# Kernel tuning notes

Hardware: AMD Instinct MI355X
Metric: run time of the kernel (lower is better)

Reference implementation:

```python
import jax, jax.numpy as jnp
import numpy as np

B, IN, HS, OUT, NBDA = 128, 64, 500, 10, 1


def setup_inputs() -> dict:
    key = jax.random.key(0)
    ks = jax.random.split(key, 16)
    inp = {
        "inputs": jax.random.normal(ks[0], (B, IN), jnp.float32),
        "hidden": jax.random.normal(ks[1], (B, HS), jnp.float32),
        "hebb": jax.random.uniform(ks[2], (B, HS, HS), jnp.float32),
        "et": jax.random.uniform(ks[3], (B, HS, HS), jnp.float32),
        "pw": jax.random.uniform(ks[4], (B, HS, HS), jnp.float32),
        # parameters (xavier-ish scale for linears, matching torch init magnitudes)
        "i2h_w": jax.random.normal(ks[5], (HS, IN), jnp.float32) * (1.0 / np.sqrt(IN)),
        "i2h_b": jnp.zeros((HS,), jnp.float32),
        "w": 0.01 * jax.random.uniform(ks[6], (HS, HS), jnp.float32),
        "alpha": 0.01 * jax.random.uniform(ks[7], (HS, HS), jnp.float32),
        "eta": 0.1 * jnp.ones((1,), jnp.float32),
        "etaet": 0.1 * jnp.ones((1,), jnp.float32),
        "h2DA_w": jax.random.normal(ks[8], (NBDA, HS), jnp.float32) * (1.0 / np.sqrt(HS)),
        "h2DA_b": jnp.zeros((NBDA,), jnp.float32),
        "h2o_w": jax.random.normal(ks[9], (OUT, HS), jnp.float32) * (1.0 / np.sqrt(HS)),
        "h2o_b": jnp.zeros((OUT,), jnp.float32),
        "h2v_w": jax.random.normal(ks[10], (1, HS), jnp.float32) * (1.0 / np.sqrt(HS)),
        "h2v_b": jnp.zeros((1,), jnp.float32),
    }
    return inp


def reference(inputs, hidden, hebb, et, pw,
              i2h_w, i2h_b, w, alpha, eta, etaet,
              h2DA_w, h2DA_b, h2o_w, h2o_b, h2v_w, h2v_b):
    # hactiv = tanh(i2h(x) + (w + alpha*pw) @ hidden)   [B,HS]
    pre = inputs @ i2h_w.T + i2h_b                       # [B,HS]
    rec = jnp.einsum('bij,bj->bi', w[None] + alpha[None] * pw, hidden)
    hactiv = jnp.tanh(pre + rec)

    activout = hactiv @ h2o_w.T + h2o_b                  # [B,OUT]
    valueout = hactiv @ h2v_w.T + h2v_b                  # [B,1]
    DAout = jnp.tanh(hactiv @ h2DA_w.T + h2DA_b)         # [B,1] (NBDA=1)

    # outer-product Hebbian trace update
    deltahebb = hactiv[:, :, None] * hidden[:, None, :]  # [B,HS,HS]
    deltapw = DAout.reshape(-1, 1, 1) * et               # retroactive modulation
    pw_new = jnp.clip(pw + deltapw, -1.0, 1.0)           # fully_modulated=True path
    hebb_new = hebb                                      # untouched when fully modulated
    et_new = (1.0 - etaet) * et + etaet * deltahebb
    hidden_new = hactiv

    return activout, valueout, hidden_new, hebb_new, et_new, pw_new
```

## Files before the change

### kernel.cpp

```cpp
#include <hip/hip_runtime.h>
#include <math.h>

#define B   128
#define IN  64
#define HS  500
#define OUT 10

typedef float f4 __attribute__((ext_vector_type(4)));

__global__ __launch_bounds__(256)
void k_hactiv(const float* __restrict__ inputs,
              const float* __restrict__ hidden,
              const float* __restrict__ pw,
              const float* __restrict__ i2h_w,
              const float* __restrict__ i2h_b,
              const float* __restrict__ w,
              const float* __restrict__ alpha,
              float* __restrict__ hactiv,
              float* __restrict__ hidden_new)
{
    __shared__ f4 h_lds[HS / 4];
    const int b    = blockIdx.x / (HS / 4);
    const int tile = blockIdx.x % (HS / 4);
    const int lane = threadIdx.x & 63;
    const int wv   = threadIdx.x >> 6;
    const int i    = tile * 4 + wv;

    if (threadIdx.x < HS / 4)
        h_lds[threadIdx.x] = ((const f4*)(hidden + (size_t)b * HS))[threadIdx.x];
    __syncthreads();

    const f4* __restrict__ pwrow = (const f4*)(pw + ((size_t)b * HS + i) * HS);
    const f4* __restrict__ wrow  = (const f4*)(w + (size_t)i * HS);
    const f4* __restrict__ arow  = (const f4*)(alpha + (size_t)i * HS);

    float acc = 0.f;
    #pragma unroll 2
    for (int v = lane; v < HS / 4; v += 64) {
        const f4 pv  = pwrow[v];
        const f4 wv4 = wrow[v];
        const f4 av  = arow[v];
        const f4 hv  = h_lds[v];
        acc += (wv4.x + av.x * pv.x) * hv.x
             + (wv4.y + av.y * pv.y) * hv.y
             + (wv4.z + av.z * pv.z) * hv.z
             + (wv4.w + av.w * pv.w) * hv.w;
    }

    acc += inputs[b * IN + lane] * i2h_w[i * IN + lane];

    #pragma unroll
    for (int off = 32; off > 0; off >>= 1)
        acc += __shfl_down(acc, off, 64);

    if (lane == 0) {
        float v = tanhf(acc + i2h_b[i]);
        hactiv[b * HS + i]     = v;
        hidden_new[b * HS + i] = v;
    }
}

__global__ __launch_bounds__(256)
void k_heads(const float* __restrict__ hactiv,
             const float* __restrict__ h2o_w,
             const float* __restrict__ h2o_b,
             const float* __restrict__ h2v_w,
             const float* __restrict__ h2v_b,
             const float* __restrict__ h2DA_w,
             const float* __restrict__ h2DA_b,
             float* __restrict__ activout,
             float* __restrict__ valueout,
             float* __restrict__ DAout)
{
    __shared__ float h_lds[HS];
    const int b    = blockIdx.x;
    const int lane = threadIdx.x & 63;
    const int wv   = threadIdx.x >> 6;

    for (int j = threadIdx.x; j < HS; j += 256) h_lds[j] = hactiv[b * HS + j];
    __syncthreads();

    float acc[3] = {0.f, 0.f, 0.f};
    #pragma unroll
    for (int oo = 0; oo < 3; ++oo) {
        const int o = wv * 3 + oo;
        const float* __restrict__ wr =
            (o < OUT) ? (h2o_w + (size_t)o * HS) : ((o == OUT) ? h2v_w : h2DA_w);
        float a = 0.f;
        for (int j = lane; j < HS; j += 64) a += wr[j] * h_lds[j];
        acc[oo] = a;
    }
    #pragma unroll
    for (int off = 32; off > 0; off >>= 1) {
        #pragma unroll
        for (int oo = 0; oo < 3; ++oo)
            acc[oo] += __shfl_down(acc[oo], off, 64);
    }
    if (lane == 0) {
        #pragma unroll
        for (int oo = 0; oo < 3; ++oo) {
            const int o = wv * 3 + oo;
            if (o < OUT)          activout[b * OUT + o] = acc[oo] + h2o_b[o];
            else if (o == OUT)    valueout[b]           = acc[oo] + h2v_b[0];
            else                  DAout[b]              = tanhf(acc[oo] + h2DA_b[0]);
        }
    }
}

#define NV4 (HS * HS / 4)

__global__ __launch_bounds__(256)
void k_update(const f4* __restrict__ hebb,
              const f4* __restrict__ et,
              const f4* __restrict__ pw,
              const float* __restrict__ hactiv,
              const float* __restrict__ hidden,
              const float* __restrict__ DAout,
              const float* __restrict__ etaet_p,
              f4* __restrict__ hebb_new,
              f4* __restrict__ et_new,
              f4* __restrict__ pw_new)
{
    const int   b     = blockIdx.y;
    const float etaet = etaet_p[0];
    const float omete = 1.f - etaet;
    const float da    = DAout[b];
    const size_t base = (size_t)b * NV4;

    const float* __restrict__ harow = hactiv + (size_t)b * HS;
    const f4*    __restrict__ hrow  = (const f4*)(hidden + (size_t)b * HS);

    const int stride = gridDim.x * blockDim.x;
    for (int v = blockIdx.x * blockDim.x + threadIdx.x; v < NV4; v += stride) {
        const int i  = v / (HS / 4);
        const int j4 = v - i * (HS / 4);

        const float ha = harow[i] * etaet;
        const f4 hj = hrow[j4];
        const f4 e  = __builtin_nontemporal_load(et + base + v);
        const f4 p  = pw[base + v];
        const f4 hb = __builtin_nontemporal_load(hebb + base + v);

        f4 en, pn;
        en.x = omete * e.x + ha * hj.x;
        en.y = omete * e.y + ha * hj.y;
        en.z = omete * e.z + ha * hj.z;
        en.w = omete * e.w + ha * hj.w;

        pn.x = fminf(fmaxf(p.x + da * e.x, -1.f), 1.f);
        pn.y = fminf(fmaxf(p.y + da * e.y, -1.f), 1.f);
        pn.z = fminf(fmaxf(p.z + da * e.z, -1.f), 1.f);
        pn.w = fminf(fmaxf(p.w + da * e.w, -1.f), 1.f);

        __builtin_nontemporal_store(hb, hebb_new + base + v);
        __builtin_nontemporal_store(en, et_new + base + v);
        __builtin_nontemporal_store(pn, pw_new + base + v);
    }
}

extern "C" void kernel_launch(void* const* d_in, const int* in_sizes, int n_in,
                              void* d_out, int out_size, void* d_ws, size_t ws_size,
                              hipStream_t stream) {
    const float* inputs  = (const float*)d_in[0];
    const float* hidden  = (const float*)d_in[1];
    const float* hebb    = (const float*)d_in[2];
    const float* et      = (const float*)d_in[3];
    const float* pw      = (const float*)d_in[4];
    const float* i2h_w   = (const float*)d_in[5];
    const float* i2h_b   = (const float*)d_in[6];
    const float* w       = (const float*)d_in[7];
    const float* alpha   = (const float*)d_in[8];
    const float* etaet   = (const float*)d_in[10];
    const float* h2DA_w  = (const float*)d_in[11];
    const float* h2DA_b  = (const float*)d_in[12];
    const float* h2o_w   = (const float*)d_in[13];
    const float* h2o_b   = (const float*)d_in[14];
    const float* h2v_w   = (const float*)d_in[15];
    const float* h2v_b   = (const float*)d_in[16];

    float* out = (float*)d_out;
    float* activout   = out;
    float* valueout   = out + B * OUT;
    float* hidden_new = out + B * OUT + B;
    float* hebb_new   = out + B * OUT + B + B * HS;
    float* et_new     = hebb_new + (size_t)B * HS * HS;
    float* pw_new     = et_new + (size_t)B * HS * HS;

    float* hactiv = (float*)d_ws;
    float* DAout  = hactiv + B * HS;

    k_hactiv<<<B * (HS / 4), 256, 0, stream>>>(
        inputs, hidden, pw, i2h_w, i2h_b, w, alpha, hactiv, hidden_new);

    k_heads<<<B, 256, 0, stream>>>(
        hactiv, h2o_w, h2o_b, h2v_w, h2v_b, h2DA_w, h2DA_b,
        activout, valueout, DAout);

    k_update<<<dim3(32, B), 256, 0, stream>>>(
        (const f4*)hebb, (const f4*)et, (const f4*)pw,
        hactiv, hidden, DAout, etaet,
        (f4*)hebb_new, (f4*)et_new, (f4*)pw_new);
}
```

Measured before the change: 664.3 us.

## Move hebb copy into hactiv kernel and process two vectors per thread in update

The pass-through copy of hebb into hebb_new moves from the update kernel into the hactiv kernel, where each block copies a fixed slice before its reduction. The aim is to overlap that pure-bandwidth traffic with the latency-bound matvec kernel. The update kernel now handles two float4 elements per thread with half the grid and uses plain instead of nontemporal loads and stores. Risks are that the copy adds bandwidth pressure to the hactiv kernel, and that dropping the nontemporal hints may change cache behaviour.

Result: slower. 688.7 us (+3.7%).

```diff
diff --git a/kernel.cpp b/kernel.cpp
--- a/kernel.cpp
+++ b/kernel.cpp
@@ -7,6 +7,10 @@
 #define OUT 10
 
 typedef float f4 __attribute__((ext_vector_type(4)));
+
+#define NBLK1   (B * (HS / 4))
+#define HEBB_F4 (B * HS * HS / 4)
+#define COPY_PER_BLK (HEBB_F4 / NBLK1)
 
 __global__ __launch_bounds__(256)
 void k_hactiv(const float* __restrict__ inputs,
@@ -16,6 +20,8 @@
               const float* __restrict__ i2h_b,
               const float* __restrict__ w,
               const float* __restrict__ alpha,
+              const f4*    __restrict__ hebb,
+              f4*          __restrict__ hebb_new,
               float* __restrict__ hactiv,
               float* __restrict__ hidden_new)
 {
@@ -28,6 +34,17 @@
 
     if (threadIdx.x < HS / 4)
         h_lds[threadIdx.x] = ((const f4*)(hidden + (size_t)b * HS))[threadIdx.x];
+
+    {
+        const size_t cbase = (size_t)blockIdx.x * COPY_PER_BLK;
+        #pragma unroll
+        for (int t = 0; t < COPY_PER_BLK / 256 + 1; ++t) {
+            const int idx = t * 256 + threadIdx.x;
+            if (idx < COPY_PER_BLK)
+                hebb_new[cbase + idx] = hebb[cbase + idx];
+        }
+    }
+
     __syncthreads();
 
     const f4* __restrict__ pwrow = (const f4*)(pw + ((size_t)b * HS + i) * HS);
@@ -108,16 +125,15 @@
 }
 
 #define NV4 (HS * HS / 4)
+#define NP2 (NV4 / 2)
 
 __global__ __launch_bounds__(256)
-void k_update(const f4* __restrict__ hebb,
-              const f4* __restrict__ et,
+void k_update(const f4* __restrict__ et,
               const f4* __restrict__ pw,
               const float* __restrict__ hactiv,
               const float* __restrict__ hidden,
               const float* __restrict__ DAout,
               const float* __restrict__ etaet_p,
-              f4* __restrict__ hebb_new,
               f4* __restrict__ et_new,
               f4* __restrict__ pw_new)
 {
@@ -131,30 +147,46 @@
     const f4*    __restrict__ hrow  = (const f4*)(hidden + (size_t)b * HS);
 
     const int stride = gridDim.x * blockDim.x;
-    for (int v = blockIdx.x * blockDim.x + threadIdx.x; v < NV4; v += stride) {
-        const int i  = v / (HS / 4);
-        const int j4 = v - i * (HS / 4);
-
-        const float ha = harow[i] * etaet;
-        const f4 hj = hrow[j4];
-        const f4 e  = __builtin_nontemporal_load(et + base + v);
-        const f4 p  = pw[base + v];
-        const f4 hb = __builtin_nontemporal_load(hebb + base + v);
-
-        f4 en, pn;
-        en.x = omete * e.x + ha * hj.x;
-        en.y = omete * e.y + ha * hj.y;
-        en.z = omete * e.z + ha * hj.z;
-        en.w = omete * e.w + ha * hj.w;
-
-        pn.x = fminf(fmaxf(p.x + da * e.x, -1.f), 1.f);
-        pn.y = fminf(fmaxf(p.y + da * e.y, -1.f), 1.f);
-        pn.z = fminf(fmaxf(p.z + da * e.z, -1.f), 1.f);
-        pn.w = fminf(fmaxf(p.w + da * e.w, -1.f), 1.f);
-
-        __builtin_nontemporal_store(hb, hebb_new + base + v);
-        __builtin_nontemporal_store(en, et_new + base + v);
-        __builtin_nontemporal_store(pn, pw_new + base + v);
+    for (int p2 = blockIdx.x * blockDim.x + threadIdx.x; p2 < NP2; p2 += stride) {
+        const int v0 = 2 * p2;
+        const int v1 = v0 + 1;
+        const int i0 = v0 / (HS / 4);
+        const int j0 = v0 - i0 * (HS / 4);
+        const int i1 = v1 / (HS / 4);
+        const int j1 = v1 - i1 * (HS / 4);
+
+        const f4 e0 = et[base + v0];
+        const f4 e1 = et[base + v1];
+        const f4 p0 = pw[base + v0];
+        const f4 p1 = pw[base + v1];
+        const float ha0 = harow[i0] * etaet;
+        const float ha1 = harow[i1] * etaet;
+        const f4 hj0 = hrow[j0];
+        const f4 hj1 = hrow[j1];
+
+        f4 en0, en1, pn0, pn1;
+        en0.x = omete * e0.x + ha0 * hj0.x;
+        en0.y = omete * e0.y + ha0 * hj0.y;
+        en0.z = omete * e0.z + ha0 * hj0.z;
+        en0.w = omete * e0.w + ha0 * hj0.w;
+        en1.x = omete * e1.x + ha1 * hj1.x;
+        en1.y = omete * e1.y + ha1 * hj1.y;
+        en1.z = omete * e1.z + ha1 * hj1.z;
+        en1.w = omete * e1.w + ha1 * hj1.w;
+
+        pn0.x = fminf(fmaxf(p0.x + da * e0.x, -1.f), 1.f);
+        pn0.y = fminf(fmaxf(p0.y + da * e0.y, -1.f), 1.f);
+        pn0.z = fminf(fmaxf(p0.z + da * e0.z, -1.f), 1.f);
+        pn0.w = fminf(fmaxf(p0.w + da * e0.w, -1.f), 1.f);
+        pn1.x = fminf(fmaxf(p1.x + da * e1.x, -1.f), 1.f);
+        pn1.y = fminf(fmaxf(p1.y + da * e1.y, -1.f), 1.f);
+        pn1.z = fminf(fmaxf(p1.z + da * e1.z, -1.f), 1.f);
+        pn1.w = fminf(fmaxf(p1.w + da * e1.w, -1.f), 1.f);
+
+        et_new[base + v0] = en0;
+        et_new[base + v1] = en1;
+        pw_new[base + v0] = pn0;
+        pw_new[base + v1] = pn1;
     }
 }
 
@@ -189,15 +221,16 @@
     float* hactiv = (float*)d_ws;
     float* DAout  = hactiv + B * HS;
 
-    k_hactiv<<<B * (HS / 4), 256, 0, stream>>>(
-        inputs, hidden, pw, i2h_w, i2h_b, w, alpha, hactiv, hidden_new);
+    k_hactiv<<<NBLK1, 256, 0, stream>>>(
+        inputs, hidden, pw, i2h_w, i2h_b, w, alpha,
+        (const f4*)hebb, (f4*)hebb_new, hactiv, hidden_new);
 
     k_heads<<<B, 256, 0, stream>>>(
         hactiv, h2o_w, h2o_b, h2v_w, h2v_b, h2DA_w, h2DA_b,
         activout, valueout, DAout);
 
-    k_update<<<dim3(32, B), 256, 0, stream>>>(
-        (const f4*)hebb, (const f4*)et, (const f4*)pw,
+    k_update<<<dim3(16, B), 256, 0, stream>>>(
+        (const f4*)et, (const f4*)pw,
         hactiv, hidden, DAout, etaet,
-        (f4*)hebb_new, (f4*)et_new, (f4*)pw_new);
-}
+        (f4*)et_new, (f4*)pw_new);
+}
```
